# Kernel tuning notes

Hardware: AMD Instinct MI355X
Metric: run time of the kernel (lower is better)

The kernel has to match this reference:

```python
import jax, jax.numpy as jnp
import numpy as np

N_NODES = 50000
N_EDGES = 800000
IN_DIM = 256
HID = 64
HEADS = [4, 4, 1]
N_CLASSES = 16
SLOPE = 0.2


def mish(x):
    return x * jnp.tanh(jax.nn.softplus(x))


def gat_conv(x, src, dst, W, attn_l, attn_r, bias, res_W, n_heads, d_out, act):
    """DGL GATConv (feat_drop=attn_drop=0, residual=True, bias=True).
    x: (N, F_in); src/dst: (E,) edge endpoints; message flows src -> dst.
    """
    N = x.shape[0]
    feat = (x @ W).reshape(N, n_heads, d_out)            # (N, H, D)
    el = jnp.sum(feat * attn_l, axis=-1)                 # (N, H)
    er = jnp.sum(feat * attn_r, axis=-1)                 # (N, H)
    e = jax.nn.leaky_relu(el[src] + er[dst], SLOPE)      # (E, H)
    # segment softmax over incoming edges of each dst node
    emax = jax.ops.segment_max(e, dst, num_segments=N)   # (N, H)
    ee = jnp.exp(e - emax[dst])                          # (E, H)
    denom = jax.ops.segment_sum(ee, dst, num_segments=N) # (N, H)
    a = ee / denom[dst]                                  # (E, H)
    # weighted scatter-aggregate of source features
    rst = jax.ops.segment_sum(feat[src] * a[:, :, None], dst, num_segments=N)  # (N, H, D)
    # residual: identity if F_in == H*D else linear projection (DGL semantics)
    if res_W is None:
        res = x.reshape(N, n_heads, d_out)
    else:
        res = (x @ res_W).reshape(N, n_heads, d_out)
    rst = rst + res + bias.reshape(1, n_heads, d_out)
    if act:
        rst = mish(rst)
    return rst


def setup_inputs() -> dict:
    key = jax.random.key(0)
    ks = jax.random.split(key, 16)
    x = jax.random.normal(ks[0], (N_NODES, IN_DIM), dtype=jnp.float32)
    src = jax.random.randint(ks[1], (N_EDGES,), 0, N_NODES, dtype=jnp.int32)
    dst = jax.random.randint(ks[2], (N_EDGES,), 0, N_NODES, dtype=jnp.int32)
    s = 0.1
    # layer 0: 256 -> 4 heads x 64
    W0 = jax.random.normal(ks[3], (IN_DIM, HEADS[0] * HID), jnp.float32) * s
    al0 = jax.random.normal(ks[4], (HEADS[0], HID), jnp.float32) * s
    ar0 = jax.random.normal(ks[5], (HEADS[0], HID), jnp.float32) * s
    b0 = jnp.zeros((HEADS[0] * HID,), jnp.float32)
    # layer 1: 256 -> 4 heads x 64
    W1 = jax.random.normal(ks[6], (HEADS[0] * HID, HEADS[1] * HID), jnp.float32) * s
    al1 = jax.random.normal(ks[7], (HEADS[1], HID), jnp.float32) * s
    ar1 = jax.random.normal(ks[8], (HEADS[1], HID), jnp.float32) * s
    b1 = jnp.zeros((HEADS[1] * HID,), jnp.float32)
    # output layer: 256 -> 1 head x 16 (residual needs a linear projection)
    W2 = jax.random.normal(ks[9], (HEADS[1] * HID, HEADS[2] * N_CLASSES), jnp.float32) * s
    al2 = jax.random.normal(ks[10], (HEADS[2], N_CLASSES), jnp.float32) * s
    ar2 = jax.random.normal(ks[11], (HEADS[2], N_CLASSES), jnp.float32) * s
    b2 = jnp.zeros((HEADS[2] * N_CLASSES,), jnp.float32)
    resW2 = jax.random.normal(ks[12], (HEADS[1] * HID, HEADS[2] * N_CLASSES), jnp.float32) * s
    return {"x": x, "src": src, "dst": dst,
            "W0": W0, "al0": al0, "ar0": ar0, "b0": b0,
            "W1": W1, "al1": al1, "ar1": ar1, "b1": b1,
            "W2": W2, "al2": al2, "ar2": ar2, "b2": b2, "resW2": resW2}


def reference(x, src, dst, W0, al0, ar0, b0, W1, al1, ar1, b1, W2, al2, ar2, b2, resW2):
    N = x.shape[0]
    h = gat_conv(x, src, dst, W0, al0, ar0, b0, None, HEADS[0], HID, True).reshape(N, -1)
    h = gat_conv(h, src, dst, W1, al1, ar1, b1, None, HEADS[1], HID, True).reshape(N, -1)
    logits = gat_conv(h, src, dst, W2, al2, ar2, b2, resW2, HEADS[2], N_CLASSES, False).mean(axis=1)
    return logits
```

## Files before the change

kernel.cpp:

```cpp
#include <hip/hip_runtime.h>
#include <cmath>
#include <type_traits>

typedef __bf16 bf16;
typedef __attribute__((ext_vector_type(8))) __bf16 bf16x8;
typedef __attribute__((ext_vector_type(4))) __bf16 bf16x4;
typedef __attribute__((ext_vector_type(4))) float f32x4;

__device__ __forceinline__ unsigned f2s(float x) {
    unsigned u = __float_as_uint(x);
    return (u & 0x80000000u) ? ~u : (u | 0x80000000u);
}
__device__ __forceinline__ float s2f(unsigned s) {
    return (s & 0x80000000u) ? __uint_as_float(s & 0x7FFFFFFFu)
                             : __uint_as_float(~s);
}

__device__ __forceinline__ float fast_mish(float x) {
    const float t = __expf(fminf(x, 32.f));
    const float num = fmaf(t, t, t + t);
    const float den = num + 2.f;
    return x * num * __builtin_amdgcn_rcpf(den);
}

__global__ void prep_weights_kernel(const float* __restrict__ W0, const float* __restrict__ W1,
                                    const float* __restrict__ W2, const float* __restrict__ rW2,
                                    bf16* __restrict__ Wt0, bf16* __restrict__ Wt1,
                                    bf16* __restrict__ Bct) {
    const int idx = blockIdx.x * blockDim.x + threadIdx.x;
    if (idx < 65536) {
        const int k = idx >> 8, m = idx & 255;
        Wt0[m * 256 + k] = (bf16)W0[idx];
        Wt1[m * 256 + k] = (bf16)W1[idx];
    }
    if (idx < 8192) {
        const int m = idx >> 8, k = idx & 255;
        const float v = (m < 16) ? W2[k * 16 + m] : rW2[k * 16 + (m - 16)];
        Bct[idx] = (bf16)v;
    }
}

template <typename AT>
__global__ __launch_bounds__(256) void gemm_mfma_bf16(const AT* __restrict__ A,
                                                      const bf16* __restrict__ Bt,
                                                      bf16* __restrict__ Fb,
                                                      const float* __restrict__ al,
                                                      const float* __restrict__ ar,
                                                      float* __restrict__ el,
                                                      float* __restrict__ er,
                                                      float* __restrict__ blockmax, int N) {
    constexpr int K = 256, BM = 128, BK = 32;
    constexpr int LDA = BK + 8;
    __shared__ bf16 As[BM * LDA];
    __shared__ bf16 Bs[BM * LDA];
    __shared__ float smax[4];

    const int tid = threadIdx.x;
    const int wave = tid >> 6, lane = tid & 63;
    const int quad = lane >> 4, l16 = lane & 15;
    const int rowBase = blockIdx.y * BM;
    const int colBase = blockIdx.x * BM;
    const int m_base = (wave >> 1) * 64, n_base = (wave & 1) * 64;

    f32x4 acc[4][4] = {};

    const int sr = tid >> 1;
    const int seg = (tid & 1) << 4;

    for (int k0 = 0; k0 < K; k0 += BK) {
        {
            const int gr = rowBase + sr;
            if constexpr (std::is_same<AT, float>::value) {
                float4 f0 = {0,0,0,0}, f1 = {0,0,0,0}, f2 = {0,0,0,0}, f3 = {0,0,0,0};
                if (gr < N) {
                    const float4* Ag = (const float4*)(A + (long)gr * K + k0 + seg);
                    f0 = Ag[0]; f1 = Ag[1]; f2 = Ag[2]; f3 = Ag[3];
                }
                bf16x8 p0, p1;
                p0[0] = (bf16)f0.x; p0[1] = (bf16)f0.y; p0[2] = (bf16)f0.z; p0[3] = (bf16)f0.w;
                p0[4] = (bf16)f1.x; p0[5] = (bf16)f1.y; p0[6] = (bf16)f1.z; p0[7] = (bf16)f1.w;
                p1[0] = (bf16)f2.x; p1[1] = (bf16)f2.y; p1[2] = (bf16)f2.z; p1[3] = (bf16)f2.w;
                p1[4] = (bf16)f3.x; p1[5] = (bf16)f3.y; p1[6] = (bf16)f3.z; p1[7] = (bf16)f3.w;
                *(bf16x8*)&As[sr * LDA + seg] = p0;
                *(bf16x8*)&As[sr * LDA + seg + 8] = p1;
            } else {
                bf16x8 p0 = {}, p1 = {};
                if (gr < N) {
                    const bf16x8* Ag = (const bf16x8*)(A + (long)gr * K + k0 + seg);
                    p0 = Ag[0]; p1 = Ag[1];
                }
                *(bf16x8*)&As[sr * LDA + seg] = p0;
                *(bf16x8*)&As[sr * LDA + seg + 8] = p1;
            }
        }
        {
            const bf16x8* Bg = (const bf16x8*)(Bt + (long)(colBase + sr) * K + k0 + seg);
            *(bf16x8*)&Bs[sr * LDA + seg] = Bg[0];
            *(bf16x8*)&Bs[sr * LDA + seg + 8] = Bg[1];
        }
        __syncthreads();

        bf16x8 af[4], bfr[4];
#pragma unroll
        for (int mi = 0; mi < 4; mi++)
            af[mi] = *(const bf16x8*)&As[(m_base + mi * 16 + l16) * LDA + quad * 8];
#pragma unroll
        for (int ni = 0; ni < 4; ni++)
            bfr[ni] = *(const bf16x8*)&Bs[(n_base + ni * 16 + l16) * LDA + quad * 8];
#pragma unroll
        for (int mi = 0; mi < 4; mi++)
#pragma unroll
            for (int ni = 0; ni < 4; ni++)
                acc[mi][ni] = __builtin_amdgcn_mfma_f32_16x16x32_bf16(af[mi], bfr[ni], acc[mi][ni], 0, 0, 0);
        __syncthreads();
    }

#pragma unroll
    for (int mi = 0; mi < 4; mi++) {
#pragma unroll
        for (int r = 0; r < 4; r++) {
            const int grow = rowBase + m_base + mi * 16 + quad * 4 + r;
            if (grow < N) {
#pragma unroll
                for (int ni = 0; ni < 4; ni++) {
                    Fb[(long)grow * 256 + colBase + n_base + ni * 16 + l16] = (bf16)acc[mi][ni][r];
                }
            }
        }
    }

    {
        const int h = (colBase >> 6) + (wave & 1);
        float alv[4], arv[4];
#pragma unroll
        for (int ni = 0; ni < 4; ni++) {
            alv[ni] = al[h * 64 + ni * 16 + l16];
            arv[ni] = ar[h * 64 + ni * 16 + l16];
        }
        float mxl = -INFINITY;
#pragma unroll
        for (int mi = 0; mi < 4; mi++) {
#pragma unroll
            for (int r = 0; r < 4; r++) {
                float sl = fmaf(acc[mi][0][r], alv[0], fmaf(acc[mi][1][r], alv[1],
                           fmaf(acc[mi][2][r], alv[2], acc[mi][3][r] * alv[3])));
                float sr2 = fmaf(acc[mi][0][r], arv[0], fmaf(acc[mi][1][r], arv[1],
                            fmaf(acc[mi][2][r], arv[2], acc[mi][3][r] * arv[3])));
#pragma unroll
                for (int off = 1; off < 16; off <<= 1) {
                    sl += __shfl_xor(sl, off);
                    sr2 += __shfl_xor(sr2, off);
                }
                const int grow = rowBase + m_base + mi * 16 + quad * 4 + r;
                if (l16 == 0 && grow < N) {
                    el[grow * 4 + h] = sl;
                    er[grow * 4 + h] = sr2;
                }
                if (grow < N) mxl = fmaxf(mxl, sl);
            }
        }
        mxl = fmaxf(mxl, __shfl_xor(mxl, 16));
        mxl = fmaxf(mxl, __shfl_xor(mxl, 32));
        if (lane == 0) smax[wave] = mxl;
        __syncthreads();
        if (lane == 0 && wave < 2) {
            const int hh = (colBase >> 6) + wave;
            blockmax[hh * gridDim.y + blockIdx.y] = fmaxf(smax[wave], smax[wave + 2]);
        }
    }
}

__global__ __launch_bounds__(256) void gemm_mfma_n32(const bf16* __restrict__ A,
                                                     const bf16* __restrict__ Bt,
                                                     float* __restrict__ F2f,
                                                     float* __restrict__ F2r,
                                                     const float* __restrict__ al2,
                                                     const float* __restrict__ ar2,
                                                     float* __restrict__ el,
                                                     float* __restrict__ er,
                                                     float* __restrict__ blockmax, int N) {
    constexpr int K = 256, BM = 128, BK = 32;
    constexpr int LDA = BK + 8;
    __shared__ bf16 As[BM * LDA];
    __shared__ bf16 Bs[32 * LDA];
    __shared__ float smax[4];

    const int tid = threadIdx.x;
    const int wave = tid >> 6, lane = tid & 63;
    const int quad = lane >> 4, l16 = lane & 15;
    const int rowBase = blockIdx.x * BM;
    const int m_base = (wave >> 1) * 64, n_base = (wave & 1) * 16;

    f32x4 acc[4] = {};

    const int sr = tid >> 1;
    const int seg = (tid & 1) << 4;

    for (int k0 = 0; k0 < K; k0 += BK) {
        {
            const int gr = rowBase + sr;
            bf16x8 p0 = {}, p1 = {};
            if (gr < N) {
                const bf16x8* Ag = (const bf16x8*)(A + (long)gr * K + k0 + seg);
                p0 = Ag[0]; p1 = Ag[1];
            }
            *(bf16x8*)&As[sr * LDA + seg] = p0;
            *(bf16x8*)&As[sr * LDA + seg + 8] = p1;
        }
        if (tid < 64) {
            const int br = tid >> 1;
            const bf16x8* Bg = (const bf16x8*)(Bt + br * K + k0 + seg);
            *(bf16x8*)&Bs[br * LDA + seg] = Bg[0];
            *(bf16x8*)&Bs[br * LDA + seg + 8] = Bg[1];
        }
        __syncthreads();

        const bf16x8 bfr = *(const bf16x8*)&Bs[(n_base + l16) * LDA + quad * 8];
#pragma unroll
        for (int mi = 0; mi < 4; mi++) {
            const bf16x8 af = *(const bf16x8*)&As[(m_base + mi * 16 + l16) * LDA + quad * 8];
            acc[mi] = __builtin_amdgcn_mfma_f32_16x16x32_bf16(af, bfr, acc[mi], 0, 0, 0);
        }
        __syncthreads();
    }

    float* __restrict__ Cq = (wave & 1) ? F2r : F2f;
#pragma unroll
    for (int mi = 0; mi < 4; mi++) {
#pragma unroll
        for (int r = 0; r < 4; r++) {
            const int grow = rowBase + m_base + mi * 16 + quad * 4 + r;
            if (grow < N) Cq[(long)grow * 16 + l16] = acc[mi][r];
        }
    }

    float mxl = -INFINITY;
    if (!(wave & 1)) {
        const float alv = al2[l16], arv = ar2[l16];
#pragma unroll
        for (int mi = 0; mi < 4; mi++) {
#pragma unroll
            for (int r = 0; r < 4; r++) {
                float sl = acc[mi][r] * alv;
                float sr2 = acc[mi][r] * arv;
#pragma unroll
                for (int off = 1; off < 16; off <<= 1) {
                    sl += __shfl_xor(sl, off);
                    sr2 += __shfl_xor(sr2, off);
                }
                const int grow = rowBase + m_base + mi * 16 + quad * 4 + r;
                if (l16 == 0 && grow < N) {
                    el[grow] = sl;
                    er[grow] = sr2;
                }
                if (grow < N) mxl = fmaxf(mxl, sl);
            }
        }
    }
    mxl = fmaxf(mxl, __shfl_xor(mxl, 16));
    mxl = fmaxf(mxl, __shfl_xor(mxl, 32));
    if (lane == 0) smax[wave] = mxl;
    __syncthreads();
    if (tid == 0) blockmax[blockIdx.x] = fmaxf(smax[0], smax[2]);
}

__global__ void reduce_blockmax_kernel(const float* __restrict__ bm, int cnt, int nheads,
                                       unsigned* __restrict__ elmax_dst) {
    const int w = threadIdx.x >> 6;
    const int lane = threadIdx.x & 63;
    if (w >= nheads) return;
    float m = -INFINITY;
    for (int i = lane; i < cnt; i += 64) m = fmaxf(m, bm[w * cnt + i]);
#pragma unroll
    for (int off = 1; off < 64; off <<= 1) m = fmaxf(m, __shfl_xor(m, off));
    if (lane == 0) elmax_dst[w] = f2s(m);
}

__global__ void count_deg_kernel(const int* __restrict__ dst, int* __restrict__ deg,
                                 int* __restrict__ pos, int E) {
    const int e = blockIdx.x * blockDim.x + threadIdx.x;
    if (e >= E) return;
    pos[e] = atomicAdd(&deg[dst[e]], 1);
}

__global__ void scan_block_kernel(const int* __restrict__ deg, int* __restrict__ scanned,
                                  int* __restrict__ block_sums, int N) {
    __shared__ int smem[256];
    const int tid = threadIdx.x;
    const int base = blockIdx.x * 1024 + tid * 4;
    int v[4];
#pragma unroll
    for (int i = 0; i < 4; i++) v[i] = (base + i < N) ? deg[base + i] : 0;
    const int tsum = v[0] + v[1] + v[2] + v[3];
    smem[tid] = tsum;
    __syncthreads();
    int acc = tsum;
    for (int off = 1; off < 256; off <<= 1) {
        const int t = (tid >= off) ? smem[tid - off] : 0;
        __syncthreads();
        acc += t;
        smem[tid] = acc;
        __syncthreads();
    }
    if (tid == 255) block_sums[blockIdx.x] = acc;
    int run = acc - tsum;
#pragma unroll
    for (int i = 0; i < 4; i++) {
        if (base + i < N) scanned[base + i] = run;
        run += v[i];
    }
}

__global__ void scan_sums_kernel(int* __restrict__ block_sums, unsigned* __restrict__ elmax_u, int nb) {
    const int tid = threadIdx.x;
    if (tid < 12) elmax_u[tid] = f2s(-INFINITY);
    const int orig = (tid < nb) ? block_sums[tid] : 0;
    int v = orig;
#pragma unroll
    for (int off = 1; off < 64; off <<= 1) {
        const int t = __shfl_up(v, off);
        if (tid >= off) v += t;
    }
    if (tid < nb) block_sums[tid] = v - orig;
}

__global__ void apply_offsets_kernel(const int* __restrict__ scanned, const int* __restrict__ block_sums,
                                     int* __restrict__ row_ptr, int N, int E) {
    const int i = blockIdx.x * blockDim.x + threadIdx.x;
    if (i < N) row_ptr[i] = scanned[i] + block_sums[i >> 10];
    if (i == 0) row_ptr[N] = E;
}

__global__ void scatter_kernel(const int* __restrict__ src, const int* __restrict__ dst,
                               const int* __restrict__ row_ptr, const int* __restrict__ pos,
                               int* __restrict__ csr_src, int E) {
    const int e = blockIdx.x * blockDim.x + threadIdx.x;
    if (e >= E) return;
    csr_src[row_ptr[dst[e]] + pos[e]] = src[e];
}

template <int H, int D, bool ACT, typename RT, typename OT>
__global__ void gat_aggregate_wave(const int* __restrict__ row_ptr, const int* __restrict__ csr_src,
                                   const float* __restrict__ el, const float* __restrict__ er,
                                   const unsigned* __restrict__ elmax_u,
                                   const bf16* __restrict__ feat,
                                   const RT* __restrict__ res, const float* __restrict__ bias,
                                   OT* __restrict__ out, int N) {
    static_assert(H == 4 && D == 64, "layout hardcoded for C=256");
    const int wave = threadIdx.x >> 6;
    const int lane = threadIdx.x & 63;
    int n = blockIdx.x * (blockDim.x >> 6) + wave;
    if (n >= N) return;
    n = __builtin_amdgcn_readfirstlane(n);
    const int sel = lane >> 5;
    const int hl = lane & 31;
    const int h = hl >> 3;

    const float erd = er[n * H + h];
    float sh = s2f(elmax_u[h]) + erd;
    sh = fmaxf(sh, 0.2f * sh);
    constexpr float L2E = 1.4426950408889634f;
    const float C1 = (erd - sh) * L2E;
    const float C2 = fmaf(0.2f, erd, -sh) * L2E;

    const char* csrB = (const char*)csr_src;
    const char* elB = (const char*)el;
    const char* featB = (const char*)feat;
    const unsigned hoff = (unsigned)(h << 2);
    const unsigned coff = (unsigned)(hl << 4);
    const unsigned selo = (unsigned)(sel << 2);

    float acc[8] = {0.f, 0.f, 0.f, 0.f, 0.f, 0.f, 0.f, 0.f};
    float l = 0.f;
    int p = row_ptr[n];
    const int pend = row_ptr[n + 1];

#define CSRLD(PP) (*(const int*)(csrB + ((unsigned)((PP) << 2) + selo)))
#define ELLD(S)   (*(const float*)(elB + ((unsigned)((S) << 4) + hoff)))
#define FTLD(S)   (*(const bf16x8*)(featB + ((unsigned)((S) << 9) + coff)))
#define WCOMP(EV) __builtin_amdgcn_exp2f(fmaxf(fmaf((EV), L2E, C1), fmaf((EV), 0.2f * L2E, C2)))

    for (; p + 8 <= pend; p += 8) {
        const int sA = CSRLD(p);
        const int sB = CSRLD(p + 2);
        const int sC = CSRLD(p + 4);
        const int sD = CSRLD(p + 6);
        const float eA = ELLD(sA);
        const float eB = ELLD(sB);
        const float eC = ELLD(sC);
        const float eD = ELLD(sD);
        const bf16x8 fA = FTLD(sA);
        const bf16x8 fB = FTLD(sB);
        const bf16x8 fC = FTLD(sC);
        const bf16x8 fD = FTLD(sD);
        const float wA = WCOMP(eA);
        const float wB = WCOMP(eB);
        const float wC = WCOMP(eC);
        const float wD = WCOMP(eD);
        l += (wA + wB) + (wC + wD);
#pragma unroll
        for (int i = 0; i < 8; i++)
            acc[i] = fmaf(wA, (float)fA[i],
                     fmaf(wB, (float)fB[i],
                     fmaf(wC, (float)fC[i],
                     fmaf(wD, (float)fD[i], acc[i]))));
    }
    for (; p + 4 <= pend; p += 4) {
        const int sA = CSRLD(p);
        const int sB = CSRLD(p + 2);
        const float eA = ELLD(sA);
        const float eB = ELLD(sB);
        const bf16x8 fA = FTLD(sA);
        const bf16x8 fB = FTLD(sB);
        const float wA = WCOMP(eA);
        const float wB = WCOMP(eB);
        l += wA + wB;
#pragma unroll
        for (int i = 0; i < 8; i++)
            acc[i] = fmaf(wA, (float)fA[i], fmaf(wB, (float)fB[i], acc[i]));
    }
    for (; p + 2 <= pend; p += 2) {
        const int sA = CSRLD(p);
        const float eA = ELLD(sA);
        const bf16x8 fA = FTLD(sA);
        const float wA = WCOMP(eA);
        l += wA;
#pragma unroll
        for (int i = 0; i < 8; i++)
            acc[i] = fmaf(wA, (float)fA[i], acc[i]);
    }
    if (p < pend) {
        const int s_ = *(const int*)(csrB + (unsigned)(p << 2));
        const float ev_ = ELLD(s_);
        float w_ = WCOMP(ev_);
        if (sel) w_ = 0.f;
        const bf16x8 f_ = FTLD(s_);
        l += w_;
#pragma unroll
        for (int i_ = 0; i_ < 8; i_++) acc[i_] = fmaf(w_, (float)f_[i_], acc[i_]);
    }
#undef CSRLD
#undef ELLD
#undef FTLD
#undef WCOMP

    l += __shfl_xor(l, 32);
#pragma unroll
    for (int i = 0; i < 8; i++) acc[i] += __shfl_xor(acc[i], 32);
    const float inv = (l > 0.f) ? __builtin_amdgcn_rcpf(l) : 0.f;

    const float a0 = (sel ? acc[4] : acc[0]) * inv;
    const float a1 = (sel ? acc[5] : acc[1]) * inv;
    const float a2 = (sel ? acc[6] : acc[2]) * inv;
    const float a3 = (sel ? acc[7] : acc[3]) * inv;
    const unsigned ib = (unsigned)(sel << 2);

    float4 r;
    if constexpr (std::is_same<RT, float>::value) {
        r = *(const float4*)((const char*)res + ((size_t)n << 10) + (coff << 1) + (ib << 2));
    } else {
        const bf16x4 rb = *(const bf16x4*)((const char*)res + ((size_t)n << 9) + coff + (ib << 1));
        r = make_float4((float)rb[0], (float)rb[1], (float)rb[2], (float)rb[3]);
    }
    const float4 bb = *(const float4*)((const char*)bias + (coff << 1) + (ib << 2));
    float v0 = a0 + r.x + bb.x;
    float v1 = a1 + r.y + bb.y;
    float v2 = a2 + r.z + bb.z;
    float v3 = a3 + r.w + bb.w;
    if (ACT) {
        v0 = fast_mish(v0);
        v1 = fast_mish(v1);
        v2 = fast_mish(v2);
        v3 = fast_mish(v3);
    }
    if constexpr (std::is_same<OT, float>::value) {
        float4 o = {v0, v1, v2, v3};
        *(float4*)((char*)out + ((size_t)n << 10) + (coff << 1) + (ib << 2)) = o;
    } else {
        bf16x4 o;
        o[0] = (bf16)v0; o[1] = (bf16)v1; o[2] = (bf16)v2; o[3] = (bf16)v3;
        *(bf16x4*)((char*)out + ((size_t)n << 9) + coff + (ib << 1)) = o;
    }
}

__global__ void gat_aggregate_small16(const int* __restrict__ row_ptr, const int* __restrict__ csr_src,
                                      const float* __restrict__ el, const float* __restrict__ er,
                                      const unsigned* __restrict__ elmax_u,
                                      const float* __restrict__ F2f, const float* __restrict__ F2r,
                                      const float* __restrict__ bias,
                                      float* __restrict__ out, int N) {
    const int wave = threadIdx.x >> 6;
    const int lane = threadIdx.x & 63;
    int n = blockIdx.x * (blockDim.x >> 6) + wave;
    if (n >= N) return;
    n = __builtin_amdgcn_readfirstlane(n);
    const int slot = lane >> 4;
    const int c = lane & 15;

    const float mx = fmaxf(fmaxf(s2f(elmax_u[8]), s2f(elmax_u[9])),
                           fmaxf(s2f(elmax_u[10]), s2f(elmax_u[11])));
    const float erd = er[n];
    float sh = mx + erd;
    sh = fmaxf(sh, 0.2f * sh);
    constexpr float L2E = 1.4426950408889634f;
    const float C1 = (erd - sh) * L2E;
    const float C2 = fmaf(0.2f, erd, -sh) * L2E;

    const char* csrB = (const char*)csr_src;
    const char* elB = (const char*)el;
    const char* fB = (const char*)F2f;
    const unsigned co = (unsigned)(c << 2);
    const unsigned so = (unsigned)(slot << 2);

    float acc = 0.f, l = 0.f;
    int p = row_ptr[n];
    const int pend = row_ptr[n + 1];
    for (; p + 8 <= pend; p += 8) {
        const int s0 = *(const int*)(csrB + ((unsigned)(p << 2) + so));
        const int s1 = *(const int*)(csrB + ((unsigned)((p + 4) << 2) + so));
        const float e0 = *(const float*)(elB + (unsigned)(s0 << 2));
        const float e1 = *(const float*)(elB + (unsigned)(s1 << 2));
        const float f0 = *(const float*)(fB + ((unsigned)(s0 << 6) + co));
        const float f1 = *(const float*)(fB + ((unsigned)(s1 << 6) + co));
        const float w0 = __builtin_amdgcn_exp2f(
            fmaxf(fmaf(e0, L2E, C1), fmaf(e0, 0.2f * L2E, C2)));
        const float w1 = __builtin_amdgcn_exp2f(
            fmaxf(fmaf(e1, L2E, C1), fmaf(e1, 0.2f * L2E, C2)));
        l += w0 + w1;
        acc = fmaf(w0, f0, fmaf(w1, f1, acc));
    }
    for (; p + 4 <= pend; p += 4) {
        const int s_ = *(const int*)(csrB + ((unsigned)(p << 2) + so));
        const float ev_ = *(const float*)(elB + (unsigned)(s_ << 2));
        const float w_ = __builtin_amdgcn_exp2f(
            fmaxf(fmaf(ev_, L2E, C1), fmaf(ev_, 0.2f * L2E, C2)));
        const float f_ = *(const float*)(fB + ((unsigned)(s_ << 6) + co));
        l += w_;
        acc = fmaf(w_, f_, acc);
    }
    if (p < pend) {
        const int q = p + slot;
        const bool valid = q < pend;
        const int qi = valid ? q : p;
        const int s_ = *(const int*)(csrB + (unsigned)(qi << 2));
        const float ev_ = *(const float*)(elB + (unsigned)(s_ << 2));
        float w_ = __builtin_amdgcn_exp2f(
            fmaxf(fmaf(ev_, L2E, C1), fmaf(ev_, 0.2f * L2E, C2)));
        if (!valid) w_ = 0.f;
        const float f_ = *(const float*)(fB + ((unsigned)(s_ << 6) + co));
        l += w_;
        acc = fmaf(w_, f_, acc);
    }
    l += __shfl_xor(l, 16);
    l += __shfl_xor(l, 32);
    acc += __shfl_xor(acc, 16);
    acc += __shfl_xor(acc, 32);
    const float inv = (l > 0.f) ? __builtin_amdgcn_rcpf(l) : 0.f;
    if (lane < 16) {
        const float rv = F2r[(long)n * 16 + c];
        out[(long)n * 16 + c] = fmaf(acc, inv, rv + bias[c]);
    }
}


static inline int cdiv(long a, long b) { return (int)((a + b - 1) / b); }

extern "C" void kernel_launch(void* const* d_in, const int* in_sizes, int n_in,
                              void* d_out, int out_size, void* d_ws, size_t ws_size,
                              hipStream_t stream) {
    const float* x   = (const float*)d_in[0];
    const int*   src = (const int*)d_in[1];
    const int*   dst = (const int*)d_in[2];
    const float* W0  = (const float*)d_in[3];
    const float* al0 = (const float*)d_in[4];
    const float* ar0 = (const float*)d_in[5];
    const float* b0  = (const float*)d_in[6];
    const float* W1  = (const float*)d_in[7];
    const float* al1 = (const float*)d_in[8];
    const float* ar1 = (const float*)d_in[9];
    const float* b1  = (const float*)d_in[10];
    const float* W2  = (const float*)d_in[11];
    const float* al2 = (const float*)d_in[12];
    const float* ar2 = (const float*)d_in[13];
    const float* b2  = (const float*)d_in[14];
    const float* rW2 = (const float*)d_in[15];
    float* out = (float*)d_out;

    const int N = in_sizes[0] / 256;
    const int E = in_sizes[1];

    bf16* Wt0    = (bf16*)d_ws;
    bf16* Wt1    = Wt0 + 65536;
    bf16* Bct    = Wt1 + 65536;
    bf16* Fb     = Bct + 8192;
    bf16* Hb     = Fb + (long)N * 256;
    float* F2f   = (float*)(Hb + (long)N * 256);
    float* F2r   = F2f + (long)N * 16;
    float* el    = F2r + (long)N * 16;
    float* er    = el + (long)N * 4;
    unsigned* elmax_u = (unsigned*)(er + (long)N * 4);
    int* deg     = (int*)(elmax_u + 12);
    int* scanned = deg + N;
    int* bsums   = scanned + N;
    int* row_ptr = bsums + 64;
    int* pos     = row_ptr + N + 1;
    int* csr_src = pos + E;
    float* bmax  = (float*)(csr_src + E);

    const int THREADS = 256;
    const int NB = cdiv(N, 1024);
    const int NBY = cdiv(N, 128);
    dim3 mfma_grid(2, NBY);

    prep_weights_kernel<<<cdiv(65536, THREADS), THREADS, 0, stream>>>(W0, W1, W2, rW2, Wt0, Wt1, Bct);
    hipMemsetAsync(deg, 0, (size_t)N * 4, stream);
    count_deg_kernel<<<cdiv(E, THREADS), THREADS, 0, stream>>>(dst, deg, pos, E);
    scan_block_kernel<<<NB, 256, 0, stream>>>(deg, scanned, bsums, N);
    scan_sums_kernel<<<1, 64, 0, stream>>>(bsums, elmax_u, NB);
    apply_offsets_kernel<<<cdiv(N, THREADS), THREADS, 0, stream>>>(scanned, bsums, row_ptr, N, E);
    scatter_kernel<<<cdiv(E, THREADS), THREADS, 0, stream>>>(src, dst, row_ptr, pos, csr_src, E);

    gemm_mfma_bf16<float><<<mfma_grid, 256, 0, stream>>>(x, Wt0, Fb, al0, ar0, el, er, bmax, N);
    reduce_blockmax_kernel<<<1, 256, 0, stream>>>(bmax, NBY, 4, elmax_u);
    gat_aggregate_wave<4, 64, true, float, bf16><<<cdiv(N, 4), 256, 0, stream>>>(
        row_ptr, csr_src, el, er, elmax_u, Fb, x, b0, Hb, N);

    gemm_mfma_bf16<bf16><<<mfma_grid, 256, 0, stream>>>(Hb, Wt1, Fb, al1, ar1, el, er, bmax, N);
    reduce_blockmax_kernel<<<1, 256, 0, stream>>>(bmax, NBY, 4, elmax_u + 4);
    gat_aggregate_wave<4, 64, true, bf16, bf16><<<cdiv(N, 4), 256, 0, stream>>>(
        row_ptr, csr_src, el, er, elmax_u + 4, Fb, Hb, b1, Hb, N);

    gemm_mfma_n32<<<cdiv(N, 128), 256, 0, stream>>>(Hb, Bct, F2f, F2r, al2, ar2, el, er, bmax, N);
    reduce_blockmax_kernel<<<1, 64, 0, stream>>>(bmax, NBY, 1, elmax_u + 8);
    gat_aggregate_small16<<<cdiv(N, 4), 256, 0, stream>>>(row_ptr, csr_src, el, er, elmax_u,
                                                          F2f, F2r, b2, out, N);
}
```

Measured before the change: 406.0 us.

## Widen GEMM tile to full 256 columns and fold deg memset into prep

The bf16 MFMA GEMM now uses 512-thread blocks that each cover a 128x256 output tile, so the A rows are loaded and converted once rather than by two column blocks. This halves the number of blocks and removes the duplicate A traffic, at the cost of larger shared memory and fewer concurrent blocks. The degree memset moves into the weight-prep kernel to drop one launch, and the last aggregation reads only the single head's max instead of four.

After: 390.0 us. 3.9% less time.

```diff
diff --git a/kernel.cpp b/kernel.cpp
--- a/kernel.cpp
+++ b/kernel.cpp
@@ -26,7 +26,7 @@
 __global__ void prep_weights_kernel(const float* __restrict__ W0, const float* __restrict__ W1,
                                     const float* __restrict__ W2, const float* __restrict__ rW2,
                                     bf16* __restrict__ Wt0, bf16* __restrict__ Wt1,
-                                    bf16* __restrict__ Bct) {
+                                    bf16* __restrict__ Bct, int* __restrict__ deg, int N) {
     const int idx = blockIdx.x * blockDim.x + threadIdx.x;
     if (idx < 65536) {
         const int k = idx >> 8, m = idx & 255;
@@ -38,10 +38,11 @@
         const float v = (m < 16) ? W2[k * 16 + m] : rW2[k * 16 + (m - 16)];
         Bct[idx] = (bf16)v;
     }
+    if (idx < N) deg[idx] = 0;
 }
 
 template <typename AT>
-__global__ __launch_bounds__(256) void gemm_mfma_bf16(const AT* __restrict__ A,
+__global__ __launch_bounds__(512) void gemm_mfma_bf16(const AT* __restrict__ A,
                                                       const bf16* __restrict__ Bt,
                                                       bf16* __restrict__ Fb,
                                                       const float* __restrict__ al,
@@ -49,54 +50,48 @@
                                                       float* __restrict__ el,
                                                       float* __restrict__ er,
                                                       float* __restrict__ blockmax, int N) {
-    constexpr int K = 256, BM = 128, BK = 32;
+    constexpr int K = 256, BM = 128, BN = 256, BK = 32;
     constexpr int LDA = BK + 8;
     __shared__ bf16 As[BM * LDA];
-    __shared__ bf16 Bs[BM * LDA];
-    __shared__ float smax[4];
+    __shared__ bf16 Bs[BN * LDA];
+    __shared__ float smax[8];
 
     const int tid = threadIdx.x;
     const int wave = tid >> 6, lane = tid & 63;
     const int quad = lane >> 4, l16 = lane & 15;
-    const int rowBase = blockIdx.y * BM;
-    const int colBase = blockIdx.x * BM;
-    const int m_base = (wave >> 1) * 64, n_base = (wave & 1) * 64;
+    const int rowBase = blockIdx.x * BM;
+    const int m_base = (wave >> 2) * 64, n_base = (wave & 3) * 64;
 
     f32x4 acc[4][4] = {};
 
-    const int sr = tid >> 1;
-    const int seg = (tid & 1) << 4;
+    const int sr = tid >> 2;
+    const int sg = (tid & 3) << 3;
+    const int br = tid >> 1;
+    const int bg = (tid & 1) << 4;
 
     for (int k0 = 0; k0 < K; k0 += BK) {
         {
             const int gr = rowBase + sr;
             if constexpr (std::is_same<AT, float>::value) {
-                float4 f0 = {0,0,0,0}, f1 = {0,0,0,0}, f2 = {0,0,0,0}, f3 = {0,0,0,0};
+                float4 f0 = {0,0,0,0}, f1 = {0,0,0,0};
                 if (gr < N) {
-                    const float4* Ag = (const float4*)(A + (long)gr * K + k0 + seg);
-                    f0 = Ag[0]; f1 = Ag[1]; f2 = Ag[2]; f3 = Ag[3];
+                    const float4* Ag = (const float4*)(A + (long)gr * K + k0 + sg);
+                    f0 = Ag[0]; f1 = Ag[1];
                 }
-                bf16x8 p0, p1;
-                p0[0] = (bf16)f0.x; p0[1] = (bf16)f0.y; p0[2] = (bf16)f0.z; p0[3] = (bf16)f0.w;
-                p0[4] = (bf16)f1.x; p0[5] = (bf16)f1.y; p0[6] = (bf16)f1.z; p0[7] = (bf16)f1.w;
-                p1[0] = (bf16)f2.x; p1[1] = (bf16)f2.y; p1[2] = (bf16)f2.z; p1[3] = (bf16)f2.w;
-                p1[4] = (bf16)f3.x; p1[5] = (bf16)f3.y; p1[6] = (bf16)f3.z; p1[7] = (bf16)f3.w;
-                *(bf16x8*)&As[sr * LDA + seg] = p0;
-                *(bf16x8*)&As[sr * LDA + seg + 8] = p1;
+                bf16x8 p;
+                p[0] = (bf16)f0.x; p[1] = (bf16)f0.y; p[2] = (bf16)f0.z; p[3] = (bf16)f0.w;
+                p[4] = (bf16)f1.x; p[5] = (bf16)f1.y; p[6] = (bf16)f1.z; p[7] = (bf16)f1.w;
+                *(bf16x8*)&As[sr * LDA + sg] = p;
             } else {
-                bf16x8 p0 = {}, p1 = {};
-                if (gr < N) {
-                    const bf16x8* Ag = (const bf16x8*)(A + (long)gr * K + k0 + seg);
-                    p0 = Ag[0]; p1 = Ag[1];
-                }
-                *(bf16x8*)&As[sr * LDA + seg] = p0;
-                *(bf16x8*)&As[sr * LDA + seg + 8] = p1;
+                bf16x8 p = {};
+                if (gr < N) p = *(const bf16x8*)(A + (long)gr * K + k0 + sg);
+                *(bf16x8*)&As[sr * LDA + sg] = p;
             }
         }
         {
-            const bf16x8* Bg = (const bf16x8*)(Bt + (long)(colBase + sr) * K + k0 + seg);
-            *(bf16x8*)&Bs[sr * LDA + seg] = Bg[0];
-            *(bf16x8*)&Bs[sr * LDA + seg + 8] = Bg[1];
+            const bf16x8* Bg = (const bf16x8*)(Bt + (long)br * K + k0 + bg);
+            *(bf16x8*)&Bs[br * LDA + bg] = Bg[0];
+            *(bf16x8*)&Bs[br * LDA + bg + 8] = Bg[1];
         }
         __syncthreads();
 
@@ -123,14 +118,14 @@
             if (grow < N) {
 #pragma unroll
                 for (int ni = 0; ni < 4; ni++) {
-                    Fb[(long)grow * 256 + colBase + n_base + ni * 16 + l16] = (bf16)acc[mi][ni][r];
+                    Fb[(long)grow * 256 + n_base + ni * 16 + l16] = (bf16)acc[mi][ni][r];
                 }
             }
         }
     }
 
     {
-        const int h = (colBase >> 6) + (wave & 1);
+        const int h = wave & 3;
         float alv[4], arv[4];
 #pragma unroll
         for (int ni = 0; ni < 4; ni++) {
@@ -163,9 +158,8 @@
         mxl = fmaxf(mxl, __shfl_xor(mxl, 32));
         if (lane == 0) smax[wave] = mxl;
         __syncthreads();
-        if (lane == 0 && wave < 2) {
-            const int hh = (colBase >> 6) + wave;
-            blockmax[hh * gridDim.y + blockIdx.y] = fmaxf(smax[wave], smax[wave + 2]);
+        if (lane == 0 && wave < 4) {
+            blockmax[wave * gridDim.x + blockIdx.x] = fmaxf(smax[wave], smax[wave + 4]);
         }
     }
 }
@@ -497,8 +491,7 @@
     const int slot = lane >> 4;
     const int c = lane & 15;
 
-    const float mx = fmaxf(fmaxf(s2f(elmax_u[8]), s2f(elmax_u[9])),
-                           fmaxf(s2f(elmax_u[10]), s2f(elmax_u[11])));
+    const float mx = s2f(elmax_u[8]);
     const float erd = er[n];
     float sh = mx + erd;
     sh = fmaxf(sh, 0.2f * sh);
@@ -610,22 +603,20 @@
     const int THREADS = 256;
     const int NB = cdiv(N, 1024);
     const int NBY = cdiv(N, 128);
-    dim3 mfma_grid(2, NBY);
-
-    prep_weights_kernel<<<cdiv(65536, THREADS), THREADS, 0, stream>>>(W0, W1, W2, rW2, Wt0, Wt1, Bct);
-    hipMemsetAsync(deg, 0, (size_t)N * 4, stream);
+
+    prep_weights_kernel<<<cdiv(65536, THREADS), THREADS, 0, stream>>>(W0, W1, W2, rW2, Wt0, Wt1, Bct, deg, N);
     count_deg_kernel<<<cdiv(E, THREADS), THREADS, 0, stream>>>(dst, deg, pos, E);
     scan_block_kernel<<<NB, 256, 0, stream>>>(deg, scanned, bsums, N);
     scan_sums_kernel<<<1, 64, 0, stream>>>(bsums, elmax_u, NB);
     apply_offsets_kernel<<<cdiv(N, THREADS), THREADS, 0, stream>>>(scanned, bsums, row_ptr, N, E);
     scatter_kernel<<<cdiv(E, THREADS), THREADS, 0, stream>>>(src, dst, row_ptr, pos, csr_src, E);
 
-    gemm_mfma_bf16<float><<<mfma_grid, 256, 0, stream>>>(x, Wt0, Fb, al0, ar0, el, er, bmax, N);
+    gemm_mfma_bf16<float><<<NBY, 512, 0, stream>>>(x, Wt0, Fb, al0, ar0, el, er, bmax, N);
     reduce_blockmax_kernel<<<1, 256, 0, stream>>>(bmax, NBY, 4, elmax_u);
     gat_aggregate_wave<4, 64, true, float, bf16><<<cdiv(N, 4), 256, 0, stream>>>(
         row_ptr, csr_src, el, er, elmax_u, Fb, x, b0, Hb, N);
 
-    gemm_mfma_bf16<bf16><<<mfma_grid, 256, 0, stream>>>(Hb, Wt1, Fb, al1, ar1, el, er, bmax, N);
+    gemm_mfma_bf16<bf16><<<NBY, 512, 0, stream>>>(Hb, Wt1, Fb, al1, ar1, el, er, bmax, N);
     reduce_blockmax_kernel<<<1, 256, 0, stream>>>(bmax, NBY, 4, elmax_u + 4);
     gat_aggregate_wave<4, 64, true, bf16, bf16><<<cdiv(N, 4), 256, 0, stream>>>(
         row_ptr, csr_src, el, er, elmax_u + 4, Fb, Hb, b1, Hb, N);
```
